# Kernel optimization log

Hardware: AMD Instinct MI355X
Metric: run time of the kernel (lower is better)

The kernel has to match this reference:

```python
import jax, jax.numpy as jnp
import numpy as np

N = 50000   # nodes
E = 600000  # edges (avg degree 12)
D = 128     # feature dim (input_dim == output_dim for residual)
G = 8       # graphs in batch
EPS = 1e-5


def setup_inputs() -> dict:
    key = jax.random.key(0)
    ks = jax.random.split(key, 8)
    x = jax.random.normal(ks[0], (N, D), dtype=jnp.float32)
    edge_index = jax.random.randint(ks[1], (2, E), 0, N)
    batch = jnp.sort(jax.random.randint(ks[2], (N,), 0, G))
    s = 1.0 / np.sqrt(D)
    Wl = jax.random.normal(ks[3], (D, D), dtype=jnp.float32) * s
    bl = jax.random.normal(ks[4], (D,), dtype=jnp.float32) * s
    Wr = jax.random.normal(ks[5], (D, D), dtype=jnp.float32) * s
    return {
        "x": x,
        "edge_index": edge_index,
        "batch": batch,
        "num_graphs": G,
        "Wl": Wl,
        "bl": bl,
        "Wr": Wr,
        "gn_weight": jnp.ones((D,), jnp.float32),
        "gn_bias": jnp.zeros((D,), jnp.float32),
        "mean_scale": jnp.ones((D,), jnp.float32),
    }


def reference(x, edge_index, batch, num_graphs, Wl, bl, Wr, gn_weight, gn_bias, mean_scale):
    n = x.shape[0]
    src, dst = edge_index[0], edge_index[1]

    # SAGEConv: mean-aggregate neighbor (source) features at target nodes
    ones_e = jnp.ones(src.shape[0], dtype=x.dtype)
    deg = jax.ops.segment_sum(ones_e, dst, num_segments=n)          # [N]
    agg = jax.ops.segment_sum(x[src], dst, num_segments=n)          # [N, D]
    agg = agg / jnp.maximum(deg, 1.0)[:, None]
    f = agg @ Wl.T + bl + x @ Wr.T                                  # lin_l(agg) + lin_r(x)

    # exact (erf) GELU, as torch F.gelu default
    f = jax.nn.gelu(f, approximate=False)

    # GraphNorm: per-graph statistics with learnable mean_scale
    ones_n = jnp.ones(n, dtype=x.dtype)
    cnt = jax.ops.segment_sum(ones_n, batch, num_segments=num_graphs)[:, None]  # [G,1]
    mean = jax.ops.segment_sum(f, batch, num_segments=num_graphs) / cnt         # [G,D]
    out = f - mean_scale * mean[batch]
    var = jax.ops.segment_sum(out * out, batch, num_segments=num_graphs) / cnt  # [G,D]
    out = out / jnp.sqrt(var[batch] + EPS) * gn_weight + gn_bias

    # dropout is identity in eval mode; residual add
    return out + x
```

## Files before the change

### kernel.cpp

```cpp
#include <hip/hip_runtime.h>
#include <hip/hip_bf16.h>

#define D 128
#define NGRAPH 8
#define EPS 1e-5f
#define CAP 48
#define BN 64

typedef __attribute__((ext_vector_type(4))) float f32x4;
typedef __attribute__((ext_vector_type(8))) short s16x8;

__device__ __forceinline__ unsigned short f2bf(float f) {
    unsigned int u = __float_as_uint(f);
    u += 0x7fffu + ((u >> 16) & 1u);
    return (unsigned short)(u >> 16);
}

__global__ __launch_bounds__(256) void prep_kernel(
    const float* __restrict__ Wl, const float* __restrict__ Wr,
    unsigned short* __restrict__ Bsw,
    const float* __restrict__ x, unsigned int* __restrict__ xb,
    const int* __restrict__ batch, int* __restrict__ bnd,
    int* __restrict__ cnt, float* __restrict__ gsum, float* __restrict__ gsumsq,
    int N)
{
    int gtid = blockIdx.x * 256 + threadIdx.x;
    int gsz  = gridDim.x * 256;
    for (int i = gtid; i < N; i += gsz) cnt[i] = 0;
    for (int i = gtid; i < 2 * NGRAPH * D; i += gsz) { gsum[i] = 0.0f; gsumsq[i] = 0.0f; }
    for (int t = gtid; t < 32768; t += gsz) {
        int j    = t & 7;
        int ln   = (t >> 3) & 63;
        int ks   = (t >> 9) & 7;
        int tile = t >> 12;
        int k = ks * 32 + (ln >> 4) * 8 + j;
        int d = tile * 16 + (ln & 15);
        float v = (k < 128) ? Wl[(size_t)d * 128 + k] : Wr[(size_t)d * 128 + (k - 128)];
        Bsw[t] = f2bf(v);
    }
    for (int i = gtid; i < N * 64; i += gsz) {
        float2 p = *(const float2*)(x + (size_t)i * 2);
        xb[i] = (unsigned int)f2bf(p.x) | ((unsigned int)f2bf(p.y) << 16);
    }
    if (gtid <= NGRAPH) {
        int g = gtid, lo = 0, hi = N;
        while (lo < hi) {
            int mid = (lo + hi) >> 1;
            if (batch[mid] < g) lo = mid + 1; else hi = mid;
        }
        bnd[g] = lo;
    }
}

__global__ __launch_bounds__(256) void fill_kernel(
    const int* __restrict__ ei, int* __restrict__ cursor,
    int* __restrict__ adj, int E)
{
    int e = blockIdx.x * 256 + threadIdx.x;
    if (e < E) {
        int dst = ei[E + e];
        int pos = atomicAdd(&cursor[dst], 1);
        if (pos < CAP) adj[(size_t)dst * CAP + pos] = ei[e];
    }
}

__global__ __launch_bounds__(256) void fused_kernel(
    const unsigned int* __restrict__ xb, const int* __restrict__ cnt,
    const int* __restrict__ adj, const unsigned short* __restrict__ Bsw,
    const float* __restrict__ bl, const int* __restrict__ batch,
    float* __restrict__ fout, float* __restrict__ gsum, float* __restrict__ gsumsq,
    int N)
{
    __shared__ unsigned short sA[BN * 256];
    int n0 = blockIdx.x * BN;
    int wave = threadIdx.x >> 6, lane = threadIdx.x & 63;

    for (int j = 0; j < 16; ++j) {
        int row  = wave * 16 + j;
        int node = n0 + row;
        float a0 = 0.0f, a1 = 0.0f;
        int deg = (node < N) ? cnt[node] : 0;
        int lim = deg < CAP ? deg : CAP;
        int v = (lane < lim) ? adj[(size_t)node * CAP + lane] : 0;
        int i = 0;
        for (; i + 4 <= lim; i += 4) {
            int nb0 = __shfl(v, i, 64),     nb1 = __shfl(v, i + 1, 64);
            int nb2 = __shfl(v, i + 2, 64), nb3 = __shfl(v, i + 3, 64);
            unsigned int u0 = xb[(size_t)nb0 * 64 + lane];
            unsigned int u1 = xb[(size_t)nb1 * 64 + lane];
            unsigned int u2 = xb[(size_t)nb2 * 64 + lane];
            unsigned int u3 = xb[(size_t)nb3 * 64 + lane];
            a0 += __uint_as_float(u0 << 16) + __uint_as_float(u1 << 16)
                + __uint_as_float(u2 << 16) + __uint_as_float(u3 << 16);
            a1 += __uint_as_float(u0 & 0xffff0000u) + __uint_as_float(u1 & 0xffff0000u)
                + __uint_as_float(u2 & 0xffff0000u) + __uint_as_float(u3 & 0xffff0000u);
        }
        for (; i < lim; ++i) {
            int nb = __shfl(v, i, 64);
            unsigned int u = xb[(size_t)nb * 64 + lane];
            a0 += __uint_as_float(u << 16);
            a1 += __uint_as_float(u & 0xffff0000u);
        }
        float inv = 1.0f / (float)(deg > 0 ? deg : 1);
        unsigned int pa = (unsigned int)f2bf(a0 * inv) | ((unsigned int)f2bf(a1 * inv) << 16);
        unsigned int px = (node < N) ? xb[(size_t)node * 64 + lane] : 0u;
        int ua = lane >> 2, wb = (lane & 3) << 2, rs = row & 31;
        *(unsigned int*)((char*)sA + row * 512 + (((ua)      ^ rs) << 4) + wb) = pa;
        *(unsigned int*)((char*)sA + row * 512 + (((ua + 16) ^ rs) << 4) + wb) = px;
    }
    __syncthreads();

    int m = lane & 15, quad = lane >> 4;
    int rl = wave * 16 + m, rs = rl & 31;
    s16x8 afrag[8];
#pragma unroll
    for (int ks = 0; ks < 8; ++ks) {
        int unit = ks * 4 + quad;
        afrag[ks] = *(const s16x8*)((char*)sA + rl * 512 + ((unit ^ rs) << 4));
    }

    int nbase = n0 + wave * 16;
    bool uni = (nbase + 15 < N) && (batch[nbase] == batch[nbase + 15]);
    int gu = (nbase < N) ? batch[nbase] : 0;

#pragma unroll
    for (int tile = 0; tile < 8; ++tile) {
        f32x4 acc = {0.0f, 0.0f, 0.0f, 0.0f};
        const s16x8* bptr = (const s16x8*)Bsw + (size_t)(tile * 8) * 64 + lane;
#pragma unroll
        for (int ks = 0; ks < 8; ++ks)
            acc = __builtin_amdgcn_mfma_f32_16x16x32_bf16(afrag[ks], bptr[(size_t)ks * 64], acc, 0, 0, 0);
        int d = tile * 16 + m;
        float bias = bl[d];
        float sm = 0.0f, sq = 0.0f;
#pragma unroll
        for (int r = 0; r < 4; ++r) {
            int node = nbase + quad * 4 + r;
            if (node < N) {
                float v = acc[r] + bias;
                float g = 0.5f * v * (1.0f + erff(v * 0.70710678118654752f));
                fout[(size_t)node * D + d] = g;
                if (uni) { sm += g; sq += g * g; }
                else {
                    int gg = batch[node];
                    unsafeAtomicAdd(&gsum[gg * D + d], g);
                    unsafeAtomicAdd(&gsumsq[gg * D + d], g * g);
                }
            }
        }
        if (uni) {
            sm += __shfl_xor(sm, 16, 64); sm += __shfl_xor(sm, 32, 64);
            sq += __shfl_xor(sq, 16, 64); sq += __shfl_xor(sq, 32, 64);
            if (quad == 0) {
                unsafeAtomicAdd(&gsum[gu * D + d], sm);
                unsafeAtomicAdd(&gsumsq[gu * D + d], sq);
            }
        }
    }
}

__global__ __launch_bounds__(256) void final_kernel(
    const float* __restrict__ f, const float* __restrict__ x,
    const int* __restrict__ batch, const int* __restrict__ bnd,
    const float* __restrict__ gsum, const float* __restrict__ gsumsq,
    const float* __restrict__ ms,
    const float* __restrict__ gw, const float* __restrict__ gb,
    float* __restrict__ out, int N)
{
    int t = blockIdx.x * 256 + threadIdx.x;
    if (t >= N * (D / 4)) return;
    int n  = t >> 5;
    int d0 = (t & 31) * 4;
    int g  = batch[n];
    int c  = bnd[g + 1] - bnd[g];
    float invc = 1.0f / (float)(c > 0 ? c : 1);
    size_t row = (size_t)n * D + d0;
    float4 fv = *(const float4*)(f + row);
    float4 xv = *(const float4*)(x + row);
    float4 s1 = *(const float4*)(gsum + g * D + d0);
    float4 s2 = *(const float4*)(gsumsq + g * D + d0);
    float4 msv = *(const float4*)(ms + d0);
    float4 gwv = *(const float4*)(gw + d0);
    float4 gbv = *(const float4*)(gb + d0);
    float4 o;
    {
        float mu = s1.x * invc, q = s2.x * invc, a = msv.x * mu;
        float sc = rsqrtf(q - 2.0f * a * mu + a * a + EPS);
        o.x = (fv.x - a) * sc * gwv.x + gbv.x + xv.x;
    }
    {
        float mu = s1.y * invc, q = s2.y * invc, a = msv.y * mu;
        float sc = rsqrtf(q - 2.0f * a * mu + a * a + EPS);
        o.y = (fv.y - a) * sc * gwv.y + gbv.y + xv.y;
    }
    {
        float mu = s1.z * invc, q = s2.z * invc, a = msv.z * mu;
        float sc = rsqrtf(q - 2.0f * a * mu + a * a + EPS);
        o.z = (fv.z - a) * sc * gwv.z + gbv.z + xv.z;
    }
    {
        float mu = s1.w * invc, q = s2.w * invc, a = msv.w * mu;
        float sc = rsqrtf(q - 2.0f * a * mu + a * a + EPS);
        o.w = (fv.w - a) * sc * gwv.w + gbv.w + xv.w;
    }
    *(float4*)(out + row) = o;
}

extern "C" void kernel_launch(void* const* d_in, const int* in_sizes, int n_in,
                              void* d_out, int out_size, void* d_ws, size_t ws_size,
                              hipStream_t stream)
{
    const float* x     = (const float*)d_in[0];
    const int*   ei    = (const int*)d_in[1];
    const int*   batch = (const int*)d_in[2];
    const float* Wl = (const float*)d_in[4];
    const float* bl = (const float*)d_in[5];
    const float* Wr = (const float*)d_in[6];
    const float* gw = (const float*)d_in[7];
    const float* gb = (const float*)d_in[8];
    const float* ms = (const float*)d_in[9];
    float* out = (float*)d_out;

    int N = in_sizes[0] / D;
    int E = in_sizes[1] / 2;
    int NBLK = (N + BN - 1) / BN;
    const int Npad = NBLK * BN;

    float*          fout = (float*)d_ws;
    unsigned int*   xb   = (unsigned int*)(fout + (size_t)Npad * D);
    unsigned short* Bsw  = (unsigned short*)(xb + (size_t)N * 64);
    float* gsum   = (float*)(Bsw + 32768);
    float* gsumsq = gsum + NGRAPH * D;
    int*   cnt    = (int*)(gsumsq + NGRAPH * D);
    int*   bnd    = cnt + N;
    int*   adj    = bnd + (NGRAPH + 1);

    prep_kernel<<<512, 256, 0, stream>>>(Wl, Wr, Bsw, x, xb, batch, bnd,
                                         cnt, gsum, gsumsq, N);

    fill_kernel<<<(E + 255) / 256, 256, 0, stream>>>(ei, cnt, adj, E);

    fused_kernel<<<NBLK, 256, 0, stream>>>(xb, cnt, adj, Bsw, bl, batch,
                                           fout, gsum, gsumsq, N);

    {
        int threads = N * (D / 4);
        final_kernel<<<(threads + 255) / 256, 256, 0, stream>>>(
            fout, x, batch, bnd, gsum, gsumsq, ms, gw, gb, out, N);
    }
}
```

Baseline: 215.0 us.

## Split aggregation from GEMM and merge prep with edge fill kernel

```diff
diff --git a/kernel.cpp b/kernel.cpp
--- a/kernel.cpp
+++ b/kernel.cpp
@@ -5,7 +5,6 @@
 #define NGRAPH 8
 #define EPS 1e-5f
 #define CAP 48
-#define BN 64
 
 typedef __attribute__((ext_vector_type(4))) float f32x4;
 typedef __attribute__((ext_vector_type(8))) short s16x8;
@@ -15,20 +14,20 @@
     u += 0x7fffu + ((u >> 16) & 1u);
     return (unsigned short)(u >> 16);
 }
-
-__global__ __launch_bounds__(256) void prep_kernel(
+__device__ __forceinline__ float blo(unsigned int u) { return __uint_as_float(u << 16); }
+__device__ __forceinline__ float bhi(unsigned int u) { return __uint_as_float(u & 0xffff0000u); }
+
+__global__ __launch_bounds__(256) void prep_fill_kernel(
     const float* __restrict__ Wl, const float* __restrict__ Wr,
     unsigned short* __restrict__ Bsw,
     const float* __restrict__ x, unsigned int* __restrict__ xb,
     const int* __restrict__ batch, int* __restrict__ bnd,
-    int* __restrict__ cnt, float* __restrict__ gsum, float* __restrict__ gsumsq,
-    int N)
-{
-    int gtid = blockIdx.x * 256 + threadIdx.x;
-    int gsz  = gridDim.x * 256;
-    for (int i = gtid; i < N; i += gsz) cnt[i] = 0;
-    for (int i = gtid; i < 2 * NGRAPH * D; i += gsz) { gsum[i] = 0.0f; gsumsq[i] = 0.0f; }
-    for (int t = gtid; t < 32768; t += gsz) {
+    const int* __restrict__ ei, int* __restrict__ cnt, int* __restrict__ adj,
+    int N, int E, int Npad, int fillB)
+{
+    int b = blockIdx.x;
+    if (b < 128) {
+        int t = b * 256 + threadIdx.x;
         int j    = t & 7;
         int ln   = (t >> 3) & 63;
         int ks   = (t >> 9) & 7;
@@ -37,89 +36,91 @@
         int d = tile * 16 + (ln & 15);
         float v = (k < 128) ? Wl[(size_t)d * 128 + k] : Wr[(size_t)d * 128 + (k - 128)];
         Bsw[t] = f2bf(v);
-    }
-    for (int i = gtid; i < N * 64; i += gsz) {
-        float2 p = *(const float2*)(x + (size_t)i * 2);
-        xb[i] = (unsigned int)f2bf(p.x) | ((unsigned int)f2bf(p.y) << 16);
-    }
-    if (gtid <= NGRAPH) {
-        int g = gtid, lo = 0, hi = N;
-        while (lo < hi) {
-            int mid = (lo + hi) >> 1;
-            if (batch[mid] < g) lo = mid + 1; else hi = mid;
-        }
-        bnd[g] = lo;
-    }
-}
-
-__global__ __launch_bounds__(256) void fill_kernel(
-    const int* __restrict__ ei, int* __restrict__ cursor,
-    int* __restrict__ adj, int E)
-{
-    int e = blockIdx.x * 256 + threadIdx.x;
-    if (e < E) {
-        int dst = ei[E + e];
-        int pos = atomicAdd(&cursor[dst], 1);
-        if (pos < CAP) adj[(size_t)dst * CAP + pos] = ei[e];
-    }
-}
-
-__global__ __launch_bounds__(256) void fused_kernel(
+    } else if (b == 128) {
+        int g = threadIdx.x;
+        if (g <= NGRAPH) {
+            int lo = 0, hi = N;
+            while (lo < hi) {
+                int mid = (lo + hi) >> 1;
+                if (batch[mid] < g) lo = mid + 1; else hi = mid;
+            }
+            bnd[g] = lo;
+        }
+    } else if (b < 129 + fillB) {
+        int e = (b - 129) * 256 + threadIdx.x;
+        if (e < E) {
+            int dst = ei[E + e];
+            int pos = atomicAdd(&cnt[dst], 1);
+            if (pos < CAP) adj[(size_t)dst * CAP + pos] = ei[e];
+        }
+    } else {
+        int iu = (b - 129 - fillB) * 256 + threadIdx.x;
+        if (iu < N * 32) {
+            float4 p = *(const float4*)(x + (size_t)iu * 4);
+            uint2 o;
+            o.x = (unsigned int)f2bf(p.x) | ((unsigned int)f2bf(p.y) << 16);
+            o.y = (unsigned int)f2bf(p.z) | ((unsigned int)f2bf(p.w) << 16);
+            *(uint2*)(xb + (size_t)iu * 2) = o;
+        } else if (iu < Npad * 32) {
+            *(uint2*)(xb + (size_t)iu * 2) = make_uint2(0u, 0u);
+        }
+    }
+}
+
+__global__ __launch_bounds__(256) void aggregate_kernel(
     const unsigned int* __restrict__ xb, const int* __restrict__ cnt,
-    const int* __restrict__ adj, const unsigned short* __restrict__ Bsw,
-    const float* __restrict__ bl, const int* __restrict__ batch,
+    const int* __restrict__ adj, unsigned int* __restrict__ Aag, int N, int Npad)
+{
+    int n = blockIdx.x * 4 + (threadIdx.x >> 6);
+    int lane = threadIdx.x & 63;
+    if (n >= Npad) return;
+    if (n >= N) { Aag[(size_t)n * 64 + lane] = 0u; return; }
+    int deg = cnt[n];
+    int lim = deg < CAP ? deg : CAP;
+    int v = (lane < lim) ? adj[(size_t)n * CAP + lane] : 0;
+    float a0 = 0.0f, a1 = 0.0f;
+    int i = 0;
+    for (; i + 8 <= lim; i += 8) {
+        int nb[8];
+#pragma unroll
+        for (int k = 0; k < 8; ++k) nb[k] = __shfl(v, i + k, 64);
+        unsigned int u[8];
+#pragma unroll
+        for (int k = 0; k < 8; ++k) u[k] = xb[(size_t)nb[k] * 64 + lane];
+#pragma unroll
+        for (int k = 0; k < 8; ++k) { a0 += blo(u[k]); a1 += bhi(u[k]); }
+    }
+    for (; i < lim; ++i) {
+        int nb = __shfl(v, i, 64);
+        unsigned int u = xb[(size_t)nb * 64 + lane];
+        a0 += blo(u); a1 += bhi(u);
+    }
+    float inv = 1.0f / (float)(deg > 0 ? deg : 1);
+    Aag[(size_t)n * 64 + lane] =
+        (unsigned int)f2bf(a0 * inv) | ((unsigned int)f2bf(a1 * inv) << 16);
+}
+
+__global__ __launch_bounds__(256) void gemm_kernel(
+    const unsigned short* __restrict__ Aag, const unsigned short* __restrict__ xb16,
+    const unsigned short* __restrict__ Bsw, const float* __restrict__ bl,
+    const int* __restrict__ batch,
     float* __restrict__ fout, float* __restrict__ gsum, float* __restrict__ gsumsq,
     int N)
 {
-    __shared__ unsigned short sA[BN * 256];
-    int n0 = blockIdx.x * BN;
     int wave = threadIdx.x >> 6, lane = threadIdx.x & 63;
-
-    for (int j = 0; j < 16; ++j) {
-        int row  = wave * 16 + j;
-        int node = n0 + row;
-        float a0 = 0.0f, a1 = 0.0f;
-        int deg = (node < N) ? cnt[node] : 0;
-        int lim = deg < CAP ? deg : CAP;
-        int v = (lane < lim) ? adj[(size_t)node * CAP + lane] : 0;
-        int i = 0;
-        for (; i + 4 <= lim; i += 4) {
-            int nb0 = __shfl(v, i, 64),     nb1 = __shfl(v, i + 1, 64);
-            int nb2 = __shfl(v, i + 2, 64), nb3 = __shfl(v, i + 3, 64);
-            unsigned int u0 = xb[(size_t)nb0 * 64 + lane];
-            unsigned int u1 = xb[(size_t)nb1 * 64 + lane];
-            unsigned int u2 = xb[(size_t)nb2 * 64 + lane];
-            unsigned int u3 = xb[(size_t)nb3 * 64 + lane];
-            a0 += __uint_as_float(u0 << 16) + __uint_as_float(u1 << 16)
-                + __uint_as_float(u2 << 16) + __uint_as_float(u3 << 16);
-            a1 += __uint_as_float(u0 & 0xffff0000u) + __uint_as_float(u1 & 0xffff0000u)
-                + __uint_as_float(u2 & 0xffff0000u) + __uint_as_float(u3 & 0xffff0000u);
-        }
-        for (; i < lim; ++i) {
-            int nb = __shfl(v, i, 64);
-            unsigned int u = xb[(size_t)nb * 64 + lane];
-            a0 += __uint_as_float(u << 16);
-            a1 += __uint_as_float(u & 0xffff0000u);
-        }
-        float inv = 1.0f / (float)(deg > 0 ? deg : 1);
-        unsigned int pa = (unsigned int)f2bf(a0 * inv) | ((unsigned int)f2bf(a1 * inv) << 16);
-        unsigned int px = (node < N) ? xb[(size_t)node * 64 + lane] : 0u;
-        int ua = lane >> 2, wb = (lane & 3) << 2, rs = row & 31;
-        *(unsigned int*)((char*)sA + row * 512 + (((ua)      ^ rs) << 4) + wb) = pa;
-        *(unsigned int*)((char*)sA + row * 512 + (((ua + 16) ^ rs) << 4) + wb) = px;
-    }
-    __syncthreads();
-
+    int row0 = blockIdx.x * 64 + wave * 16;
     int m = lane & 15, quad = lane >> 4;
-    int rl = wave * 16 + m, rs = rl & 31;
+    int r = row0 + m;
+
     s16x8 afrag[8];
-#pragma unroll
-    for (int ks = 0; ks < 8; ++ks) {
-        int unit = ks * 4 + quad;
-        afrag[ks] = *(const s16x8*)((char*)sA + rl * 512 + ((unit ^ rs) << 4));
-    }
-
-    int nbase = n0 + wave * 16;
+    const unsigned short* ab = Aag + (size_t)r * 128 + quad * 8;
+#pragma unroll
+    for (int ks = 0; ks < 4; ++ks) afrag[ks] = *(const s16x8*)(ab + ks * 32);
+    const unsigned short* xp = xb16 + (size_t)r * 128 + quad * 8;
+#pragma unroll
+    for (int ks = 0; ks < 4; ++ks) afrag[4 + ks] = *(const s16x8*)(xp + ks * 32);
+
+    int nbase = row0;
     bool uni = (nbase + 15 < N) && (batch[nbase] == batch[nbase + 15]);
     int gu = (nbase < N) ? batch[nbase] : 0;
 
@@ -134,10 +135,10 @@
         float bias = bl[d];
         float sm = 0.0f, sq = 0.0f;
 #pragma unroll
-        for (int r = 0; r < 4; ++r) {
-            int node = nbase + quad * 4 + r;
+        for (int rr = 0; rr < 4; ++rr) {
+            int node = nbase + quad * 4 + rr;
             if (node < N) {
-                float v = acc[r] + bias;
+                float v = acc[rr] + bias;
                 float g = 0.5f * v * (1.0f + erff(v * 0.70710678118654752f));
                 fout[(size_t)node * D + d] = g;
                 if (uni) { sm += g; sq += g * g; }
@@ -223,25 +224,31 @@
 
     int N = in_sizes[0] / D;
     int E = in_sizes[1] / 2;
-    int NBLK = (N + BN - 1) / BN;
-    const int Npad = NBLK * BN;
+    int NBLK = (N + 63) / 64;
+    int Npad = NBLK * 64;
 
     float*          fout = (float*)d_ws;
     unsigned int*   xb   = (unsigned int*)(fout + (size_t)Npad * D);
-    unsigned short* Bsw  = (unsigned short*)(xb + (size_t)N * 64);
+    unsigned short* Bsw  = (unsigned short*)(xb + (size_t)Npad * 64);
     float* gsum   = (float*)(Bsw + 32768);
     float* gsumsq = gsum + NGRAPH * D;
     int*   cnt    = (int*)(gsumsq + NGRAPH * D);
     int*   bnd    = cnt + N;
     int*   adj    = bnd + (NGRAPH + 1);
-
-    prep_kernel<<<512, 256, 0, stream>>>(Wl, Wr, Bsw, x, xb, batch, bnd,
-                                         cnt, gsum, gsumsq, N);
-
-    fill_kernel<<<(E + 255) / 256, 256, 0, stream>>>(ei, cnt, adj, E);
-
-    fused_kernel<<<NBLK, 256, 0, stream>>>(xb, cnt, adj, Bsw, bl, batch,
-                                           fout, gsum, gsumsq, N);
+    unsigned int* Aag = (unsigned int*)(adj + (size_t)N * CAP);
+
+    hipMemsetAsync(gsum, 0, (2 * NGRAPH * D) * sizeof(float) + (size_t)N * sizeof(int), stream);
+
+    int fillB = (E + 255) / 256;
+    int xbB   = (Npad * 32 + 255) / 256;
+    prep_fill_kernel<<<129 + fillB + xbB, 256, 0, stream>>>(
+        Wl, Wr, Bsw, x, xb, batch, bnd, ei, cnt, adj, N, E, Npad, fillB);
+
+    aggregate_kernel<<<Npad / 4, 256, 0, stream>>>(xb, cnt, adj, Aag, N, Npad);
+
+    gemm_kernel<<<NBLK, 256, 0, stream>>>(
+        (const unsigned short*)Aag, (const unsigned short*)xb, Bsw, bl, batch,
+        fout, gsum, gsumsq, N);
 
     {
         int threads = N * (D / 4);
```

Result: faster. 198.9 us (-7.5%).
